# Kernel optimization log

Hardware: AMD Instinct MI355X
Metric: run time of the kernel (lower is better)

## Reference

```python
import jax, jax.numpy as jnp
import numpy as np

S = 16384      # imwidth * imheight = 128 * 128
RANK = 64
N = 8          # number of TT cores; 6 middle cores


def setup_inputs() -> dict:
    key = jax.random.key(0)
    k1, k2, k3, k4 = jax.random.split(key, 4)
    z = jax.random.normal(k1, (S,), dtype=jnp.float32)
    # TT cores: first (1, s, r), middle (N-2, r, s, r), last (r, s, 1)
    tt_first = jax.random.normal(k2, (1, S, RANK), dtype=jnp.float32) / np.float32(np.sqrt(S))
    tt_mid = jax.random.normal(k3, (N - 2, RANK, S, RANK), dtype=jnp.float32) / np.float32(np.sqrt(S))
    tt_last = jax.random.normal(k4, (RANK, S, 1), dtype=jnp.float32) / np.float32(np.sqrt(S))
    return {"z": z, "tt_first": tt_first, "tt_mid": tt_mid, "tt_last": tt_last}


def reference(z, tt_first, tt_mid, tt_last):
    # V[k] = z contracted with core k over the s axis -> (d1, d2)
    V_mid = jnp.einsum('s,kasb->kab', z, tt_mid)   # (N-2, r, r)
    V_last = jnp.einsum('s,asb->ab', z, tt_last)   # (r, 1)
    f = tt_first[0]                                 # (s, r)
    # strictly sequential chain of small matmuls: f = f @ V[1] @ ... @ V[N-2]
    def step(f, Vk):
        return f @ Vk, None
    f, _ = jax.lax.scan(step, f, V_mid)             # (s, r)
    f = f @ V_last                                  # (s, 1)
    return f.reshape(-1)
```

## Files before the change

### kernel.cpp

```cpp
#include <hip/hip_runtime.h>

#define SDIM 16384
#define RANK 64
#define NMID 6
#define NCHUNK 8
#define CHUNK_LEN (SDIM / NCHUNK)
#define VMID_BLOCKS (NMID * RANK * NCHUNK)

__global__ __launch_bounds__(256) void k_contract(
    const float* __restrict__ z, const float* __restrict__ tt_mid,
    const float* __restrict__ tt_last, float* __restrict__ part,
    float* __restrict__ vlast) {
  if (blockIdx.x < VMID_BLOCKS) {
    const int idx = blockIdx.x;
    const int c  = idx & (NCHUNK - 1);
    const int ka = idx / NCHUNK;
    const float* __restrict__ src =
        tt_mid + ((size_t)ka * SDIM + (size_t)c * CHUNK_LEN) * RANK;
    const float* __restrict__ zz = z + (size_t)c * CHUNK_LEN;

    const int b8  = threadIdx.x & 7;
    const int row = threadIdx.x >> 3;

    float4 acc0 = {0.f, 0.f, 0.f, 0.f};
    float4 acc1 = {0.f, 0.f, 0.f, 0.f};
#pragma unroll 4
    for (int s = row; s < CHUNK_LEN; s += 32) {
      const float w = zz[s];
      const float4* p =
          reinterpret_cast<const float4*>(src + (size_t)s * RANK + b8 * 8);
      const float4 v0 = p[0];
      const float4 v1 = p[1];
      acc0.x += w * v0.x; acc0.y += w * v0.y;
      acc0.z += w * v0.z; acc0.w += w * v0.w;
      acc1.x += w * v1.x; acc1.y += w * v1.y;
      acc1.z += w * v1.z; acc1.w += w * v1.w;
    }

    __shared__ float4 lds[512];
    lds[threadIdx.x * 2]     = acc0;
    lds[threadIdx.x * 2 + 1] = acc1;
    __syncthreads();
    if (threadIdx.x < 16) {
      float4 sum = {0.f, 0.f, 0.f, 0.f};
      for (int r = 0; r < 32; ++r) {
        const float4 t = lds[r * 16 + threadIdx.x];
        sum.x += t.x; sum.y += t.y; sum.z += t.z; sum.w += t.w;
      }
      *reinterpret_cast<float4*>(
          part + ((size_t)ka * NCHUNK + c) * RANK + threadIdx.x * 4) = sum;
    }
  } else {
    const int a = blockIdx.x - VMID_BLOCKS;
    const float* __restrict__ src = tt_last + (size_t)a * SDIM;
    float acc = 0.f;
    for (int i = threadIdx.x; i < SDIM / 4; i += 256) {
      const float4 v = *reinterpret_cast<const float4*>(src + i * 4);
      const float4 w = *reinterpret_cast<const float4*>(z + i * 4);
      acc += v.x * w.x + v.y * w.y + v.z * w.z + v.w * w.w;
    }
    __shared__ float red[256];
    red[threadIdx.x] = acc;
    __syncthreads();
    for (int off = 128; off > 0; off >>= 1) {
      if (threadIdx.x < off) red[threadIdx.x] += red[threadIdx.x + off];
      __syncthreads();
    }
    if (threadIdx.x == 0) vlast[a] = red[0];
  }
}

__global__ __launch_bounds__(64) void k_fold(
    const float* __restrict__ part, float* __restrict__ V) {
  const int ka = blockIdx.x;
  const int b  = threadIdx.x;
  float s = 0.f;
#pragma unroll
  for (int c = 0; c < NCHUNK; ++c)
    s += part[((size_t)ka * NCHUNK + c) * RANK + b];
  V[(size_t)ka * RANK + b] = s;
}

__global__ __launch_bounds__(256) void k_chain_out(
    const float* __restrict__ V, const float* __restrict__ vlast,
    const float* __restrict__ tt_first, float* __restrict__ out) {
  __shared__ float su[RANK];
  __shared__ float snew[RANK];
  __shared__ float red[256];
  if (threadIdx.x < RANK) su[threadIdx.x] = vlast[threadIdx.x];
  __syncthreads();

  const int a = threadIdx.x >> 2;
  const int t = threadIdx.x & 3;
  for (int k = NMID - 1; k >= 0; --k) {
    const float* __restrict__ Vk =
        V + (size_t)k * RANK * RANK + (size_t)a * RANK + t * 16;
    float s = 0.f;
#pragma unroll
    for (int b = 0; b < 16; ++b) s += Vk[b] * su[t * 16 + b];
    red[threadIdx.x] = s;
    __syncthreads();
    if (t == 0)
      snew[a] = red[a * 4] + red[a * 4 + 1] + red[a * 4 + 2] + red[a * 4 + 3];
    __syncthreads();
    if (threadIdx.x < RANK) su[threadIdx.x] = snew[threadIdx.x];
    __syncthreads();
  }

  const int r = blockIdx.x * 16 + (threadIdx.x >> 4);
  const int j = threadIdx.x & 15;
  const float4 v =
      *reinterpret_cast<const float4*>(tt_first + (size_t)r * RANK + j * 4);
  const float4 w = *reinterpret_cast<const float4*>(su + j * 4);
  float s = v.x * w.x + v.y * w.y + v.z * w.z + v.w * w.w;
  s += __shfl_xor(s, 1, 16);
  s += __shfl_xor(s, 2, 16);
  s += __shfl_xor(s, 4, 16);
  s += __shfl_xor(s, 8, 16);
  if (j == 0) out[r] = s;
}

extern "C" void kernel_launch(void* const* d_in, const int* in_sizes, int n_in,
                              void* d_out, int out_size, void* d_ws,
                              size_t ws_size, hipStream_t stream) {
  const float* z        = (const float*)d_in[0];
  const float* tt_first = (const float*)d_in[1];
  const float* tt_mid   = (const float*)d_in[2];
  const float* tt_last  = (const float*)d_in[3];
  float* out = (float*)d_out;
  float* ws  = (float*)d_ws;

  float* part  = ws;
  float* V     = part + (size_t)NMID * RANK * NCHUNK * RANK;
  float* vlast = V + (size_t)NMID * RANK * RANK;

  k_contract<<<VMID_BLOCKS + RANK, 256, 0, stream>>>(z, tt_mid, tt_last, part, vlast);
  k_fold<<<NMID * RANK, 64, 0, stream>>>(part, V);
  k_chain_out<<<SDIM / 16, 256, 0, stream>>>(V, vlast, tt_first, out);
}
```

Measured before the change: 275.8 us.

## Stage z in LDS, use nontemporal loads, reorder blocks, batch chain rows

The contraction kernel now stages each chunk of z in shared memory and reads tt_mid with nontemporal loads. The tt_last blocks are moved to the front of the grid so they are scheduled first. The chain/output kernel processes 64 rows per block instead of 16, which cuts the grid by four and with it the redundant per-block recomputation of the 6-step vector chain. The cost is the extra LDS staging and sync, and fewer blocks for the final stage.

```diff
diff --git a/kernel.cpp b/kernel.cpp
--- a/kernel.cpp
+++ b/kernel.cpp
@@ -6,57 +6,62 @@
 #define NCHUNK 8
 #define CHUNK_LEN (SDIM / NCHUNK)
 #define VMID_BLOCKS (NMID * RANK * NCHUNK)
+#define VLAST_BLOCKS RANK
+
+typedef float float4n __attribute__((ext_vector_type(4)));
 
 __global__ __launch_bounds__(256) void k_contract(
     const float* __restrict__ z, const float* __restrict__ tt_mid,
     const float* __restrict__ tt_last, float* __restrict__ part,
     float* __restrict__ vlast) {
-  if (blockIdx.x < VMID_BLOCKS) {
-    const int idx = blockIdx.x;
+  if (blockIdx.x >= VLAST_BLOCKS) {
+    const int idx = blockIdx.x - VLAST_BLOCKS;
     const int c  = idx & (NCHUNK - 1);
     const int ka = idx / NCHUNK;
     const float* __restrict__ src =
         tt_mid + ((size_t)ka * SDIM + (size_t)c * CHUNK_LEN) * RANK;
     const float* __restrict__ zz = z + (size_t)c * CHUNK_LEN;
 
+    __shared__ float zs[CHUNK_LEN];
+#pragma unroll
+    for (int i = threadIdx.x; i < CHUNK_LEN / 4; i += 256)
+      reinterpret_cast<float4n*>(zs)[i] =
+          reinterpret_cast<const float4n*>(zz)[i];
+    __syncthreads();
+
     const int b8  = threadIdx.x & 7;
     const int row = threadIdx.x >> 3;
 
-    float4 acc0 = {0.f, 0.f, 0.f, 0.f};
-    float4 acc1 = {0.f, 0.f, 0.f, 0.f};
+    float4n acc0 = {0.f, 0.f, 0.f, 0.f};
+    float4n acc1 = {0.f, 0.f, 0.f, 0.f};
 #pragma unroll 4
     for (int s = row; s < CHUNK_LEN; s += 32) {
-      const float w = zz[s];
-      const float4* p =
-          reinterpret_cast<const float4*>(src + (size_t)s * RANK + b8 * 8);
-      const float4 v0 = p[0];
-      const float4 v1 = p[1];
-      acc0.x += w * v0.x; acc0.y += w * v0.y;
-      acc0.z += w * v0.z; acc0.w += w * v0.w;
-      acc1.x += w * v1.x; acc1.y += w * v1.y;
-      acc1.z += w * v1.z; acc1.w += w * v1.w;
+      const float w = zs[s];
+      const float4n* p =
+          reinterpret_cast<const float4n*>(src + (size_t)s * RANK + b8 * 8);
+      const float4n v0 = __builtin_nontemporal_load(p);
+      const float4n v1 = __builtin_nontemporal_load(p + 1);
+      acc0 += w * v0;
+      acc1 += w * v1;
     }
 
-    __shared__ float4 lds[512];
+    __shared__ float4n lds[512];
     lds[threadIdx.x * 2]     = acc0;
     lds[threadIdx.x * 2 + 1] = acc1;
     __syncthreads();
     if (threadIdx.x < 16) {
-      float4 sum = {0.f, 0.f, 0.f, 0.f};
-      for (int r = 0; r < 32; ++r) {
-        const float4 t = lds[r * 16 + threadIdx.x];
-        sum.x += t.x; sum.y += t.y; sum.z += t.z; sum.w += t.w;
-      }
-      *reinterpret_cast<float4*>(
+      float4n sum = {0.f, 0.f, 0.f, 0.f};
+      for (int r = 0; r < 32; ++r) sum += lds[r * 16 + threadIdx.x];
+      *reinterpret_cast<float4n*>(
           part + ((size_t)ka * NCHUNK + c) * RANK + threadIdx.x * 4) = sum;
     }
   } else {
-    const int a = blockIdx.x - VMID_BLOCKS;
+    const int a = blockIdx.x;
     const float* __restrict__ src = tt_last + (size_t)a * SDIM;
     float acc = 0.f;
     for (int i = threadIdx.x; i < SDIM / 4; i += 256) {
-      const float4 v = *reinterpret_cast<const float4*>(src + i * 4);
-      const float4 w = *reinterpret_cast<const float4*>(z + i * 4);
+      const float4n v = *reinterpret_cast<const float4n*>(src + i * 4);
+      const float4n w = *reinterpret_cast<const float4n*>(z + i * 4);
       acc += v.x * w.x + v.y * w.y + v.z * w.z + v.w * w.w;
     }
     __shared__ float red[256];
@@ -107,17 +112,20 @@
     __syncthreads();
   }
 
-  const int r = blockIdx.x * 16 + (threadIdx.x >> 4);
   const int j = threadIdx.x & 15;
-  const float4 v =
-      *reinterpret_cast<const float4*>(tt_first + (size_t)r * RANK + j * 4);
-  const float4 w = *reinterpret_cast<const float4*>(su + j * 4);
-  float s = v.x * w.x + v.y * w.y + v.z * w.z + v.w * w.w;
-  s += __shfl_xor(s, 1, 16);
-  s += __shfl_xor(s, 2, 16);
-  s += __shfl_xor(s, 4, 16);
-  s += __shfl_xor(s, 8, 16);
-  if (j == 0) out[r] = s;
+  const float4n w = *reinterpret_cast<const float4n*>(su + j * 4);
+#pragma unroll
+  for (int g = 0; g < 4; ++g) {
+    const int r = blockIdx.x * 64 + g * 16 + (threadIdx.x >> 4);
+    const float4n v =
+        *reinterpret_cast<const float4n*>(tt_first + (size_t)r * RANK + j * 4);
+    float s = v.x * w.x + v.y * w.y + v.z * w.z + v.w * w.w;
+    s += __shfl_xor(s, 1, 16);
+    s += __shfl_xor(s, 2, 16);
+    s += __shfl_xor(s, 4, 16);
+    s += __shfl_xor(s, 8, 16);
+    if (j == 0) out[r] = s;
+  }
 }
 
 extern "C" void kernel_launch(void* const* d_in, const int* in_sizes, int n_in,
@@ -134,7 +142,8 @@
   float* V     = part + (size_t)NMID * RANK * NCHUNK * RANK;
   float* vlast = V + (size_t)NMID * RANK * RANK;
 
-  k_contract<<<VMID_BLOCKS + RANK, 256, 0, stream>>>(z, tt_mid, tt_last, part, vlast);
+  k_contract<<<VLAST_BLOCKS + VMID_BLOCKS, 256, 0, stream>>>(
+      z, tt_mid, tt_last, part, vlast);
   k_fold<<<NMID * RANK, 64, 0, stream>>>(part, V);
-  k_chain_out<<<SDIM / 16, 256, 0, stream>>>(V, vlast, tt_first, out);
+  k_chain_out<<<SDIM / 64, 256, 0, stream>>>(V, vlast, tt_first, out);
 }
```

Result: slower. 295.4 us (+7.1%).
